# Performance work log

Measured on AMD Instinct MI355X. Metric: run time of the kernel, lower is better.

## Reference

```python
import jax, jax.numpy as jnp
import numpy as np
from functools import partial

DT = 0.1
EPS_RES = 0.01
EIG_MIN = 0.1
EIG_CLIP = 0.99
CHUNK = 128

B, T, D, K = 8, 4096, 1024, 256


def setup_inputs() -> dict:
    key = jax.random.key(0)
    k1, k2, k3, k4, k5 = jax.random.split(key, 5)
    x = jax.random.normal(k1, (B, T, D), dtype=jnp.float32)
    # paper init: alpha ~ U(-3, 0)
    alpha_raw = -3.0 * jax.random.uniform(k2, (K,), dtype=jnp.float32)
    # omega_k = 2*pi*k/K
    omega = 2.0 * jnp.pi * jnp.arange(K, dtype=jnp.float32) / K
    W_in = jax.random.normal(k3, (K, D), dtype=jnp.float32) / np.sqrt(D)
    W_out = jax.random.normal(k4, (D, K), dtype=jnp.float32) / np.sqrt(K)
    M = jax.random.normal(k5, (K, K), dtype=jnp.float32)
    return {"x": x, "alpha_raw": alpha_raw, "omega": omega,
            "W_in": W_in, "W_out": W_out, "M": M}


def _forward(x, alpha_raw, omega, W_in, W_out, M):
    Bb, Tt, Dd = x.shape
    Kk = alpha_raw.shape[0]
    n_chunks = Tt // CHUNK

    # eigenvalue magnitude/phase with constraints
    mag = EIG_MIN + jax.nn.sigmoid(alpha_raw) * (EIG_CLIP - EIG_MIN)     # (K,)
    cos_p = jnp.cos(omega * DT)
    sin_p = jnp.sin(omega * DT)
    # resonance R = I + eps * M / ||M||_F
    R = jnp.eye(Kk, dtype=x.dtype) + EPS_RES * M / (jnp.linalg.norm(M) + 1e-8)

    # parallel input projection for all timesteps: (B,T,K)
    beta = jnp.einsum('btd,kd->btk', x, W_in)
    # (n_chunks, CHUNK, B, K) for scanning over chunks then timesteps
    beta_c = jnp.transpose(beta.reshape(Bb, n_chunks, CHUNK, Kk), (1, 2, 0, 3))

    def time_step(carry, b):
        r, i = carry                                     # (B,K) each
        nr = b + mag * (r * cos_p - i * sin_p)           # beta added to real only
        ni = mag * (r * sin_p + i * cos_p)
        return (nr, ni), (nr, ni)

    def chunk_step(carry, beta_ch):
        # beta_ch: (CHUNK, B, K)
        (_, _), (ar, ai) = jax.lax.scan(time_step, carry, beta_ch)
        # resonance coupling applied to every state of the chunk
        ar = ar @ R
        ai = ai @ R
        # state handed to next chunk is the resonance-coupled last state,
        # detached at the chunk boundary (as in the original training scheme)
        new_carry = (jax.lax.stop_gradient(ar[-1]), jax.lax.stop_gradient(ai[-1]))
        return new_carry, ar

    zero = jnp.zeros((Bb, Kk), dtype=x.dtype)
    _, states_real = jax.lax.scan(chunk_step, (zero, zero), beta_c)
    # states_real: (n_chunks, CHUNK, B, K) -> (B, T, K)
    states_real = jnp.transpose(states_real, (2, 0, 1, 3)).reshape(Bb, Tt, Kk)

    # parallel output projection (dropout is identity in eval)
    out = jnp.einsum('btk,dk->btd', states_real, W_out)
    return out


@jax.jit
def reference(x, alpha_raw, omega, W_in, W_out, M):
    return _forward(x, alpha_raw, omega, W_in, W_out, M)
```

## Files before the change

kernel.cpp:

```cpp
#include <hip/hip_runtime.h>
#include <math.h>


typedef __attribute__((ext_vector_type(8))) short short8;
typedef __attribute__((ext_vector_type(4))) float f32x4;

#define EPS_RES 0.01f

union U8 { unsigned u[4]; short8 s8; };

__device__ __forceinline__ unsigned short f2bf(float f) {
  unsigned u = __float_as_uint(f) + 0x8000u;
  return (unsigned short)(u >> 16);
}
__device__ __forceinline__ float bf2f(unsigned short h) {
  return __uint_as_float(((unsigned)h) << 16);
}
__device__ __forceinline__ unsigned pk2bf(float f0, float f1) {
  return __builtin_amdgcn_perm(__float_as_uint(f1) + 0x8000u,
                               __float_as_uint(f0) + 0x8000u, 0x07060302u);
}
__device__ __forceinline__ void gl_lds16(const void* g, void* l) {
  __builtin_amdgcn_global_load_lds(
      (const __attribute__((address_space(1))) unsigned*)g,
      (__attribute__((address_space(3))) unsigned*)l, 16, 0, 0);
}

__global__ __launch_bounds__(256) void k_setup(const float* __restrict__ M,
                                               float* __restrict__ part,
                                               const float* __restrict__ W,
                                               unsigned short* __restrict__ o) {
  const int bid = blockIdx.x;
  if (bid < 64) {
    const int i = (bid * 256 + threadIdx.x) * 4;
    const float4 v = *(const float4*)(M + i);
    float s = v.x * v.x + v.y * v.y + v.z * v.z + v.w * v.w;
    #pragma unroll
    for (int off = 32; off > 0; off >>= 1) s += __shfl_down(s, off);
    __shared__ float red[4];
    const int lane = threadIdx.x & 63, wv = threadIdx.x >> 6;
    if (lane == 0) red[wv] = s;
    __syncthreads();
    if (threadIdx.x == 0)
      part[bid] = red[0] + red[1] + red[2] + red[3];
  } else {
    const int i = ((bid - 64) * 256 + threadIdx.x) * 4;
    float4 v = *(const float4*)(W + i);
    uint2 p;
    p.x = pk2bf(v.x, v.y);
    p.y = pk2bf(v.z, v.w);
    *(uint2*)(o + i) = p;
  }
}

__device__ __forceinline__ float norm_scale(const float* __restrict__ part) {
  float nsum = 0.f;
  #pragma unroll
  for (int i = 0; i < 64; ++i) nsum += part[i];
  return EPS_RES / (sqrtf(nsum) + 1e-8f);
}

__global__ __launch_bounds__(256) void k_wcomb(const float* __restrict__ Wout,
                                               const float* __restrict__ Mm,
                                               const float* __restrict__ npart,
                                               unsigned short* __restrict__ WcT) {
  const int d0 = blockIdx.x * 8;
  const int k = threadIdx.x;
  __shared__ float wl[8][256];
  #pragma unroll
  for (int dd = 0; dd < 8; ++dd) wl[dd][k] = Wout[(size_t)(d0 + dd) * 256 + k];
  __syncthreads();
  float acc[8] = {0.f, 0.f, 0.f, 0.f, 0.f, 0.f, 0.f, 0.f};
  const float4* Mr = (const float4*)(Mm + (size_t)k * 256);
  for (int j4 = 0; j4 < 64; ++j4) {
    const float4 m4 = Mr[j4];
    #pragma unroll
    for (int dd = 0; dd < 8; ++dd) {
      acc[dd] = fmaf(m4.x, wl[dd][j4 * 4 + 0], acc[dd]);
      acc[dd] = fmaf(m4.y, wl[dd][j4 * 4 + 1], acc[dd]);
      acc[dd] = fmaf(m4.z, wl[dd][j4 * 4 + 2], acc[dd]);
      acc[dd] = fmaf(m4.w, wl[dd][j4 * 4 + 3], acc[dd]);
    }
  }
  const float s = norm_scale(npart);
  #pragma unroll
  for (int dd = 0; dd < 8; ++dd)
    WcT[(size_t)(d0 + dd) * 256 + k] =
        f2bf(Wout[(size_t)(d0 + dd) * 256 + k] + s * acc[dd]);
}

__global__ __launch_bounds__(256) void k_gemm1(const float* __restrict__ A,
                                               const unsigned short* __restrict__ Bw,
                                               float* __restrict__ C) {
  __shared__ __align__(16) float lA[3][64 * 32];
  __shared__ __align__(16) unsigned short lB[3][256 * 32];
  const int tid = threadIdx.x;
  const int wv = tid >> 6, lane = tid & 63;
  const int m0 = blockIdx.x * 64;
  const int wn = wv;
  const int lrow = lane & 15, q = lane >> 4;

  const int a_r8 = lane >> 3;
  const int a_gl = (lane & 7) ^ a_r8;
  const int b_r16 = lane >> 2;
  const int b_gl = (lane & 3) ^ ((b_r16 >> 1) & 3);

  const float* Ab = A + (size_t)(m0 + wv * 16 + a_r8) * 1024 + a_gl * 4;
  const unsigned short* Bb = Bw + (size_t)(wv * 64 + b_r16) * 1024 + b_gl * 8;

  f32x4 acc[4][4] = {};

  auto stage = [&](int bf, int k0) {
    #pragma unroll
    for (int j = 0; j < 2; ++j)
      gl_lds16(Ab + (size_t)j * 8 * 1024 + k0,
               &lA[bf][(wv * 16 + j * 8) * 32]);
    #pragma unroll
    for (int j = 0; j < 4; ++j)
      gl_lds16(Bb + (size_t)j * 16 * 1024 + k0,
               &lB[bf][(wv * 64 + j * 16) * 32]);
  };

  auto compute = [&](int cur) {
    short8 af[4], bfv[4];
    #pragma unroll
    for (int t = 0; t < 4; ++t) {
      const int ra = t * 16 + lrow, sw = ra & 7;
      const float4 lo = *(const float4*)&lA[cur][ra * 32 + (((2 * q) ^ sw) << 2)];
      const float4 hi = *(const float4*)&lA[cur][ra * 32 + (((2 * q + 1) ^ sw) << 2)];
      U8 u;
      u.u[0] = pk2bf(lo.x, lo.y);
      u.u[1] = pk2bf(lo.z, lo.w);
      u.u[2] = pk2bf(hi.x, hi.y);
      u.u[3] = pk2bf(hi.z, hi.w);
      af[t] = u.s8;
      const int rb = wn * 64 + t * 16 + lrow;
      bfv[t] = *(const short8*)&lB[cur][rb * 32 + (q ^ ((rb >> 1) & 3)) * 8];
    }
    #pragma unroll
    for (int tm = 0; tm < 4; ++tm)
      #pragma unroll
      for (int tn = 0; tn < 4; ++tn)
        acc[tm][tn] = __builtin_amdgcn_mfma_f32_16x16x32_bf16(
            af[tm], bfv[tn], acc[tm][tn], 0, 0, 0);
  };

  stage(0, 0);
  stage(1, 32);
  int cur = 0;
  for (int j = 0; j < 31; ++j) {
    asm volatile("s_waitcnt vmcnt(6)" ::: "memory");
    __builtin_amdgcn_s_barrier();
    if (j + 2 < 32) {
      const int nx = (cur + 2 >= 3) ? cur - 1 : cur + 2;
      stage(nx, (j + 2) * 32);
    }
    compute(cur);
    cur = (cur + 1 >= 3) ? 0 : cur + 1;
  }
  asm volatile("s_waitcnt vmcnt(0)" ::: "memory");
  __builtin_amdgcn_s_barrier();
  compute(cur);

  const int rbase = m0 + q * 4;
  const int cbase = wn * 64 + lrow;
  #pragma unroll
  for (int tm = 0; tm < 4; ++tm)
    #pragma unroll
    for (int tn = 0; tn < 4; ++tn)
      #pragma unroll
      for (int r = 0; r < 4; ++r)
        C[(size_t)(rbase + tm * 16 + r) * 256 + (cbase + tn * 16)] =
            acc[tm][tn][r];
}

__global__ __launch_bounds__(256) void k_gemm2(const unsigned short* __restrict__ A,
                                               const unsigned short* __restrict__ Bw,
                                               float* __restrict__ C) {
  __shared__ __align__(16) unsigned short lA[3][128 * 32];
  __shared__ __align__(16) unsigned short lB[3][128 * 32];
  const int tid = threadIdx.x;
  const int wv = tid >> 6, lane = tid & 63;
  const int bid = blockIdx.x + (blockIdx.y << 8);
  const int xcd = bid & 7, ii = bid >> 3;
  const int m0 = ((xcd << 5) + (ii >> 3)) * 128;
  const int n0 = (ii & 7) * 128;
  const int wm = wv & 1, wn = wv >> 1;
  const int lrow = lane & 15, q = lane >> 4;

  const int r16 = lane >> 2;
  const int g4 = (lane & 3) ^ ((r16 >> 1) & 3);

  const unsigned short* Ab = A + (size_t)(m0 + wv * 32 + r16) * 256 + g4 * 8;
  const unsigned short* Bb = Bw + (size_t)(n0 + wv * 32 + r16) * 256 + g4 * 8;

  f32x4 acc[4][4] = {};

  auto stage = [&](int bf, int k0) {
    #pragma unroll
    for (int j = 0; j < 2; ++j) {
      gl_lds16(Ab + (size_t)j * 16 * 256 + k0,
               &lA[bf][(wv * 32 + j * 16) * 32]);
      gl_lds16(Bb + (size_t)j * 16 * 256 + k0,
               &lB[bf][(wv * 32 + j * 16) * 32]);
    }
  };

  auto compute = [&](int cur) {
    short8 af[4], bfv[4];
    #pragma unroll
    for (int t = 0; t < 4; ++t) {
      const int ra = wm * 64 + t * 16 + lrow;
      af[t] = *(const short8*)&lA[cur][ra * 32 + ((q ^ ((ra >> 1) & 3)) << 3)];
      const int rb = wn * 64 + t * 16 + lrow;
      bfv[t] = *(const short8*)&lB[cur][rb * 32 + ((q ^ ((rb >> 1) & 3)) << 3)];
    }
    #pragma unroll
    for (int tm = 0; tm < 4; ++tm)
      #pragma unroll
      for (int tn = 0; tn < 4; ++tn)
        acc[tm][tn] = __builtin_amdgcn_mfma_f32_16x16x32_bf16(
            af[tm], bfv[tn], acc[tm][tn], 0, 0, 0);
  };

  stage(0, 0);
  stage(1, 32);
  int cur = 0;
  for (int j = 0; j < 7; ++j) {
    asm volatile("s_waitcnt vmcnt(4)" ::: "memory");
    __builtin_amdgcn_s_barrier();
    if (j + 2 < 8) {
      const int nx = (cur + 2 >= 3) ? cur - 1 : cur + 2;
      stage(nx, (j + 2) * 32);
    }
    compute(cur);
    cur = (cur + 1 >= 3) ? 0 : cur + 1;
  }
  asm volatile("s_waitcnt vmcnt(0)" ::: "memory");
  __builtin_amdgcn_s_barrier();
  compute(cur);

  const int rbase = m0 + wm * 64 + (lane >> 4) * 4;
  const int cbase = n0 + wn * 64 + (lane & 15);
  #pragma unroll
  for (int tm = 0; tm < 4; ++tm)
    #pragma unroll
    for (int tn = 0; tn < 4; ++tn)
      #pragma unroll
      for (int r = 0; r < 4; ++r)
        C[(size_t)(rbase + tm * 16 + r) * 1024 + (cbase + tn * 16)] =
            acc[tm][tn][r];
}

__global__ __launch_bounds__(256) void k_scan(const float* __restrict__ beta,
                                              unsigned short* __restrict__ rez,
                                              float* __restrict__ lastR,
                                              float* __restrict__ lastI,
                                              const float* __restrict__ alpha_raw,
                                              const float* __restrict__ omega) {
  const int c = blockIdx.x & 31, b = blockIdx.x >> 5;
  const int k = threadIdx.x;
  const float a = alpha_raw[k];
  const float sig = 1.f / (1.f + expf(-a));
  const float mag = 0.1f + sig * (0.99f - 0.1f);
  const float om = omega[k] * 0.1f;
  const float lc = mag * cosf(om), ls = mag * sinf(om);

  const size_t m0 = (size_t)b * 4096 + (size_t)c * 128;
  const float* bp = beta + m0 * 256 + k;
  unsigned short* rp = rez + m0 * 256 + k;
  float r = 0.f, im = 0.f;
  #pragma unroll 8
  for (int t = 0; t < 128; ++t) {
    float be = bp[(size_t)t * 256];
    float nr = fmaf(lc, r, fmaf(-ls, im, be));
    float ni = fmaf(ls, r, lc * im);
    r = nr; im = ni;
    rp[(size_t)t * 256] = f2bf(r);
  }
  const int idx = (c * 8 + b) * 256 + k;
  lastR[idx] = r;
  lastI[idx] = im;
}

__global__ __launch_bounds__(256) void k_carry(const float* __restrict__ lastR,
                                               const float* __restrict__ lastI,
                                               const float* __restrict__ Mm,
                                               const float* __restrict__ npart,
                                               float* __restrict__ carR,
                                               float* __restrict__ carI) {
  const int c = blockIdx.x & 31, b = blockIdx.x >> 5;
  const int j = threadIdx.x;
  const int oidx = (c * 8 + b) * 256 + j;
  if (c == 0) {
    carR[oidx] = 0.f;
    carI[oidx] = 0.f;
    return;
  }
  __shared__ float lr[256], li[256];
  const int iidx = ((c - 1) * 8 + b) * 256;
  lr[j] = lastR[iidx + j];
  li[j] = lastI[iidx + j];
  __syncthreads();
  float ar = 0.f, ai = 0.f;
  for (int kk = 0; kk < 256; ++kk) {
    float m = Mm[(size_t)kk * 256 + j];
    ar = fmaf(lr[kk], m, ar);
    ai = fmaf(li[kk], m, ai);
  }
  const float s = norm_scale(npart);
  carR[oidx] = lr[j] + s * ar;
  carI[oidx] = li[j] + s * ai;
}

__global__ __launch_bounds__(256) void k_fixup(unsigned short* __restrict__ rez,
                                               const float* __restrict__ carR,
                                               const float* __restrict__ carI,
                                               const float* __restrict__ alpha_raw,
                                               const float* __restrict__ omega) {
  const int tg = blockIdx.x & 7;
  const int cb = blockIdx.x >> 3;
  const int b = cb & 7, c = (cb >> 3) + 1;
  const int k = threadIdx.x;
  const float a = alpha_raw[k];
  const float sig = 1.f / (1.f + expf(-a));
  const float mag = 0.1f + sig * (0.99f - 0.1f);
  const float om = omega[k] * 0.1f;
  const float l2m = log2f(mag);

  const float cr = carR[(c * 8 + b) * 256 + k];
  const float ci = carI[(c * 8 + b) * 256 + k];
  unsigned short* rp =
      rez + ((size_t)b * 4096 + (size_t)c * 128 + tg * 8) * 256 + k;
  #pragma unroll
  for (int tt = 0; tt < 8; ++tt) {
    const float tp1 = (float)(tg * 8 + tt + 1);
    const float p = exp2f(tp1 * l2m);
    const float ang = tp1 * om;
    const float hr = p * (cosf(ang) * cr - sinf(ang) * ci);
    rp[(size_t)tt * 256] = f2bf(bf2f(rp[(size_t)tt * 256]) + hr);
  }
}

extern "C" void kernel_launch(void* const* d_in, const int* in_sizes, int n_in,
                              void* d_out, int out_size, void* d_ws,
                              size_t ws_size, hipStream_t stream) {
  const float* x         = (const float*)d_in[0];
  const float* alpha_raw = (const float*)d_in[1];
  const float* omega     = (const float*)d_in[2];
  const float* W_in      = (const float*)d_in[3];
  const float* W_out     = (const float*)d_in[4];
  const float* Mm        = (const float*)d_in[5];
  float* out = (float*)d_out;

  char* ws = (char*)d_ws;
  float*          beta  = (float*)(ws);
  unsigned short* rez   = (unsigned short*)(ws + 33554432);
  float*          lastR = (float*)(ws + 50331648);
  float*          lastI = (float*)(ws + 50331648 + 262144);
  float*          carR  = (float*)(ws + 50331648 + 2 * 262144);
  float*          carI  = (float*)(ws + 50331648 + 3 * 262144);
  unsigned short* WcT   = (unsigned short*)(ws + 50331648 + 4 * 262144);
  float*          npart = (float*)(ws + 50331648 + 4 * 262144 + 524288);
  unsigned short* WinT  = (unsigned short*)d_out;

  k_setup<<<320, 256, 0, stream>>>(Mm, npart, W_in, WinT);
  k_wcomb<<<128, 256, 0, stream>>>(W_out, Mm, npart, WcT);
  k_gemm1<<<512, 256, 0, stream>>>(x, WinT, beta);
  k_scan<<<256, 256, 0, stream>>>(beta, rez, lastR, lastI, alpha_raw, omega);
  k_carry<<<256, 256, 0, stream>>>(lastR, lastI, Mm, npart, carR, carI);
  k_fixup<<<1984, 256, 0, stream>>>(rez, carR, carI, alpha_raw, omega);
  k_gemm2<<<dim3(256, 8), 256, 0, stream>>>(rez, WcT, out);
}
```

Baseline: 329.7 us.

## Load GEMM B operand directly from global and double-buffer A with wider K tiles

Both projection GEMMs stop staging the weight (B) operand through shared memory and instead read its MFMA fragments straight from global memory into registers. Only the A operand is still staged, now double-buffered with a 64-wide K slice instead of triple-buffered 32-wide slices. Synchronisation becomes a plain __syncthreads per step instead of hand-tuned vmcnt waits. This cuts LDS footprint and LDS traffic, which may raise occupancy, but exposes B global-load latency in the MFMA loop and reduces prefetch depth.

Result: no change. 334.5 us (+1.4%).

```diff
diff --git a/kernel.cpp b/kernel.cpp
--- a/kernel.cpp
+++ b/kernel.cpp
@@ -92,75 +92,65 @@
 __global__ __launch_bounds__(256) void k_gemm1(const float* __restrict__ A,
                                                const unsigned short* __restrict__ Bw,
                                                float* __restrict__ C) {
-  __shared__ __align__(16) float lA[3][64 * 32];
-  __shared__ __align__(16) unsigned short lB[3][256 * 32];
+  __shared__ __align__(16) float lA[2][64 * 64];
   const int tid = threadIdx.x;
   const int wv = tid >> 6, lane = tid & 63;
   const int m0 = blockIdx.x * 64;
   const int wn = wv;
   const int lrow = lane & 15, q = lane >> 4;
 
-  const int a_r8 = lane >> 3;
-  const int a_gl = (lane & 7) ^ a_r8;
-  const int b_r16 = lane >> 2;
-  const int b_gl = (lane & 3) ^ ((b_r16 >> 1) & 3);
-
-  const float* Ab = A + (size_t)(m0 + wv * 16 + a_r8) * 1024 + a_gl * 4;
-  const unsigned short* Bb = Bw + (size_t)(wv * 64 + b_r16) * 1024 + b_gl * 8;
+  const int s_r4 = lane >> 4;
+
+  const unsigned short* Bt[4];
+  #pragma unroll
+  for (int t = 0; t < 4; ++t)
+    Bt[t] = Bw + (size_t)(wn * 64 + t * 16 + lrow) * 1024 + q * 8;
 
   f32x4 acc[4][4] = {};
 
   auto stage = [&](int bf, int k0) {
     #pragma unroll
-    for (int j = 0; j < 2; ++j)
-      gl_lds16(Ab + (size_t)j * 8 * 1024 + k0,
-               &lA[bf][(wv * 16 + j * 8) * 32]);
-    #pragma unroll
-    for (int j = 0; j < 4; ++j)
-      gl_lds16(Bb + (size_t)j * 16 * 1024 + k0,
-               &lB[bf][(wv * 64 + j * 16) * 32]);
+    for (int j = 0; j < 4; ++j) {
+      const int rloc = j * 4 + s_r4;
+      const int g = (lane & 15) ^ rloc;
+      gl_lds16(A + (size_t)(m0 + wv * 16 + rloc) * 1024 + k0 + g * 4,
+               &lA[bf][(wv * 16 + j * 4) * 64]);
+    }
   };
 
-  auto compute = [&](int cur) {
-    short8 af[4], bfv[4];
-    #pragma unroll
-    for (int t = 0; t < 4; ++t) {
-      const int ra = t * 16 + lrow, sw = ra & 7;
-      const float4 lo = *(const float4*)&lA[cur][ra * 32 + (((2 * q) ^ sw) << 2)];
-      const float4 hi = *(const float4*)&lA[cur][ra * 32 + (((2 * q + 1) ^ sw) << 2)];
-      U8 u;
-      u.u[0] = pk2bf(lo.x, lo.y);
-      u.u[1] = pk2bf(lo.z, lo.w);
-      u.u[2] = pk2bf(hi.x, hi.y);
-      u.u[3] = pk2bf(hi.z, hi.w);
-      af[t] = u.s8;
-      const int rb = wn * 64 + t * 16 + lrow;
-      bfv[t] = *(const short8*)&lB[cur][rb * 32 + (q ^ ((rb >> 1) & 3)) * 8];
-    }
-    #pragma unroll
-    for (int tm = 0; tm < 4; ++tm)
-      #pragma unroll
-      for (int tn = 0; tn < 4; ++tn)
-        acc[tm][tn] = __builtin_amdgcn_mfma_f32_16x16x32_bf16(
-            af[tm], bfv[tn], acc[tm][tn], 0, 0, 0);
-  };
-
   stage(0, 0);
-  stage(1, 32);
-  int cur = 0;
-  for (int j = 0; j < 31; ++j) {
-    asm volatile("s_waitcnt vmcnt(6)" ::: "memory");
-    __builtin_amdgcn_s_barrier();
-    if (j + 2 < 32) {
-      const int nx = (cur + 2 >= 3) ? cur - 1 : cur + 2;
-      stage(nx, (j + 2) * 32);
-    }
-    compute(cur);
-    cur = (cur + 1 >= 3) ? 0 : cur + 1;
-  }
-  asm volatile("s_waitcnt vmcnt(0)" ::: "memory");
-  __builtin_amdgcn_s_barrier();
-  compute(cur);
+  for (int s = 0; s < 16; ++s) {
+    const int cur = s & 1;
+    __syncthreads();
+    if (s + 1 < 16) stage(cur ^ 1, (s + 1) * 64);
+
+    #pragma unroll
+    for (int ks = 0; ks < 2; ++ks) {
+      short8 af[4], bfv[4];
+      #pragma unroll
+      for (int t = 0; t < 4; ++t) {
+        const int ra = t * 16 + lrow;
+        const int g0 = ks * 8 + 2 * q;
+        const float4 lo =
+            *(const float4*)&lA[cur][ra * 64 + ((g0 ^ (ra & 15)) << 2)];
+        const float4 hi =
+            *(const float4*)&lA[cur][ra * 64 + (((g0 + 1) ^ (ra & 15)) << 2)];
+        U8 u;
+        u.u[0] = pk2bf(lo.x, lo.y);
+        u.u[1] = pk2bf(lo.z, lo.w);
+        u.u[2] = pk2bf(hi.x, hi.y);
+        u.u[3] = pk2bf(hi.z, hi.w);
+        af[t] = u.s8;
+        bfv[t] = *(const short8*)(Bt[t] + s * 64 + ks * 32);
+      }
+      #pragma unroll
+      for (int tm = 0; tm < 4; ++tm)
+        #pragma unroll
+        for (int tn = 0; tn < 4; ++tn)
+          acc[tm][tn] = __builtin_amdgcn_mfma_f32_16x16x32_bf16(
+              af[tm], bfv[tn], acc[tm][tn], 0, 0, 0);
+    }
+  }
 
   const int rbase = m0 + q * 4;
   const int cbase = wn * 64 + lrow;
@@ -177,8 +167,7 @@
 __global__ __launch_bounds__(256) void k_gemm2(const unsigned short* __restrict__ A,
                                                const unsigned short* __restrict__ Bw,
                                                float* __restrict__ C) {
-  __shared__ __align__(16) unsigned short lA[3][128 * 32];
-  __shared__ __align__(16) unsigned short lB[3][128 * 32];
+  __shared__ __align__(16) unsigned short lA[2][128 * 64];
   const int tid = threadIdx.x;
   const int wv = tid >> 6, lane = tid & 63;
   const int bid = blockIdx.x + (blockIdx.y << 8);
@@ -188,57 +177,49 @@
   const int wm = wv & 1, wn = wv >> 1;
   const int lrow = lane & 15, q = lane >> 4;
 
-  const int r16 = lane >> 2;
-  const int g4 = (lane & 3) ^ ((r16 >> 1) & 3);
-
-  const unsigned short* Ab = A + (size_t)(m0 + wv * 32 + r16) * 256 + g4 * 8;
-  const unsigned short* Bb = Bw + (size_t)(n0 + wv * 32 + r16) * 256 + g4 * 8;
+  const int s_r8 = lane >> 3;
+
+  const unsigned short* Bt[4];
+  #pragma unroll
+  for (int t = 0; t < 4; ++t)
+    Bt[t] = Bw + (size_t)(n0 + wn * 64 + t * 16 + lrow) * 256 + q * 8;
 
   f32x4 acc[4][4] = {};
 
   auto stage = [&](int bf, int k0) {
     #pragma unroll
-    for (int j = 0; j < 2; ++j) {
-      gl_lds16(Ab + (size_t)j * 16 * 256 + k0,
-               &lA[bf][(wv * 32 + j * 16) * 32]);
-      gl_lds16(Bb + (size_t)j * 16 * 256 + k0,
-               &lB[bf][(wv * 32 + j * 16) * 32]);
+    for (int j = 0; j < 4; ++j) {
+      const int rloc = j * 8 + s_r8;
+      const int g = (lane & 7) ^ (rloc & 7);
+      gl_lds16(A + (size_t)(m0 + wv * 32 + rloc) * 256 + k0 + g * 8,
+               &lA[bf][(wv * 32 + j * 8) * 64]);
     }
   };
 
-  auto compute = [&](int cur) {
-    short8 af[4], bfv[4];
-    #pragma unroll
-    for (int t = 0; t < 4; ++t) {
-      const int ra = wm * 64 + t * 16 + lrow;
-      af[t] = *(const short8*)&lA[cur][ra * 32 + ((q ^ ((ra >> 1) & 3)) << 3)];
-      const int rb = wn * 64 + t * 16 + lrow;
-      bfv[t] = *(const short8*)&lB[cur][rb * 32 + ((q ^ ((rb >> 1) & 3)) << 3)];
-    }
-    #pragma unroll
-    for (int tm = 0; tm < 4; ++tm)
-      #pragma unroll
-      for (int tn = 0; tn < 4; ++tn)
-        acc[tm][tn] = __builtin_amdgcn_mfma_f32_16x16x32_bf16(
-            af[tm], bfv[tn], acc[tm][tn], 0, 0, 0);
-  };
-
   stage(0, 0);
-  stage(1, 32);
-  int cur = 0;
-  for (int j = 0; j < 7; ++j) {
-    asm volatile("s_waitcnt vmcnt(4)" ::: "memory");
-    __builtin_amdgcn_s_barrier();
-    if (j + 2 < 8) {
-      const int nx = (cur + 2 >= 3) ? cur - 1 : cur + 2;
-      stage(nx, (j + 2) * 32);
-    }
-    compute(cur);
-    cur = (cur + 1 >= 3) ? 0 : cur + 1;
-  }
-  asm volatile("s_waitcnt vmcnt(0)" ::: "memory");
-  __builtin_amdgcn_s_barrier();
-  compute(cur);
+  for (int s = 0; s < 4; ++s) {
+    const int cur = s & 1;
+    __syncthreads();
+    if (s + 1 < 4) stage(cur ^ 1, (s + 1) * 64);
+
+    #pragma unroll
+    for (int ks = 0; ks < 2; ++ks) {
+      short8 af[4], bfv[4];
+      #pragma unroll
+      for (int t = 0; t < 4; ++t) {
+        const int ra = wm * 64 + t * 16 + lrow;
+        af[t] = *(const short8*)
+            &lA[cur][ra * 64 + (((ks * 4 + q) ^ (ra & 7)) << 3)];
+        bfv[t] = *(const short8*)(Bt[t] + s * 64 + ks * 32);
+      }
+      #pragma unroll
+      for (int tm = 0; tm < 4; ++tm)
+        #pragma unroll
+        for (int tn = 0; tn < 4; ++tn)
+          acc[tm][tn] = __builtin_amdgcn_mfma_f32_16x16x32_bf16(
+              af[tm], bfv[tn], acc[tm][tn], 0, 0, 0);
+    }
+  }
 
   const int rbase = m0 + wm * 64 + (lane >> 4) * 4;
   const int cbase = n0 + wn * 64 + (lane & 15);
```

## Fuse intra-chunk scan into input-projection GEMM epilogue via LDS staging

Applied to the files above, without the earlier changes.

The input-projection GEMM now computes 128x128 tiles, one per (batch, chunk, half-K), and stages the accumulator tile in shared memory. The first 128 threads then run the 128-step recurrence directly from LDS and write bf16 states plus the last states. This removes the separate scan kernel and the 32 MB fp32 beta round trip through global memory. In exchange the scan epilogue runs on only half the block's threads while the other half sit idle, and the larger tile changes occupancy and LDS use (72 KB per block).

New measurement: 320.0 us. 1.03x faster.

```diff
diff --git a/kernel.cpp b/kernel.cpp
--- a/kernel.cpp
+++ b/kernel.cpp
@@ -91,13 +91,18 @@
 
 __global__ __launch_bounds__(256) void k_gemm1(const float* __restrict__ A,
                                                const unsigned short* __restrict__ Bw,
-                                               float* __restrict__ C) {
-  __shared__ __align__(16) float lA[3][64 * 32];
-  __shared__ __align__(16) unsigned short lB[3][256 * 32];
+                                               unsigned short* __restrict__ rez,
+                                               float* __restrict__ lastR,
+                                               float* __restrict__ lastI,
+                                               const float* __restrict__ alpha_raw,
+                                               const float* __restrict__ omega) {
+  __shared__ __align__(16) char arena[73728];
   const int tid = threadIdx.x;
   const int wv = tid >> 6, lane = tid & 63;
-  const int m0 = blockIdx.x * 64;
-  const int wn = wv;
+  const int mt = blockIdx.x >> 1;
+  const int n0 = (blockIdx.x & 1) * 128;
+  const int m0 = mt * 128;
+  const int wm = wv & 1, wn = wv >> 1;
   const int lrow = lane & 15, q = lane >> 4;
 
   const int a_r8 = lane >> 3;
@@ -105,29 +110,33 @@
   const int b_r16 = lane >> 2;
   const int b_gl = (lane & 3) ^ ((b_r16 >> 1) & 3);
 
-  const float* Ab = A + (size_t)(m0 + wv * 16 + a_r8) * 1024 + a_gl * 4;
-  const unsigned short* Bb = Bw + (size_t)(wv * 64 + b_r16) * 1024 + b_gl * 8;
+  const float* Ab = A + (size_t)(m0 + wv * 32 + a_r8) * 1024 + a_gl * 4;
+  const unsigned short* Bb =
+      Bw + (size_t)(n0 + wv * 32 + b_r16) * 1024 + b_gl * 8;
 
   f32x4 acc[4][4] = {};
 
   auto stage = [&](int bf, int k0) {
+    float* la = (float*)(arena + bf * 16384);
+    unsigned short* lb = (unsigned short*)(arena + 49152 + bf * 8192);
+    #pragma unroll
+    for (int j = 0; j < 4; ++j)
+      gl_lds16(Ab + (size_t)j * 8 * 1024 + k0, &la[(wv * 32 + j * 8) * 32]);
     #pragma unroll
     for (int j = 0; j < 2; ++j)
-      gl_lds16(Ab + (size_t)j * 8 * 1024 + k0,
-               &lA[bf][(wv * 16 + j * 8) * 32]);
-    #pragma unroll
-    for (int j = 0; j < 4; ++j)
-      gl_lds16(Bb + (size_t)j * 16 * 1024 + k0,
-               &lB[bf][(wv * 64 + j * 16) * 32]);
+      gl_lds16(Bb + (size_t)j * 16 * 1024 + k0, &lb[(wv * 32 + j * 16) * 32]);
   };
 
   auto compute = [&](int cur) {
+    const float* la = (const float*)(arena + cur * 16384);
+    const unsigned short* lb =
+        (const unsigned short*)(arena + 49152 + cur * 8192);
     short8 af[4], bfv[4];
     #pragma unroll
     for (int t = 0; t < 4; ++t) {
-      const int ra = t * 16 + lrow, sw = ra & 7;
-      const float4 lo = *(const float4*)&lA[cur][ra * 32 + (((2 * q) ^ sw) << 2)];
-      const float4 hi = *(const float4*)&lA[cur][ra * 32 + (((2 * q + 1) ^ sw) << 2)];
+      const int ra = wm * 64 + t * 16 + lrow, sw = ra & 7;
+      const float4 lo = *(const float4*)&la[ra * 32 + (((2 * q) ^ sw) << 2)];
+      const float4 hi = *(const float4*)&la[ra * 32 + (((2 * q + 1) ^ sw) << 2)];
       U8 u;
       u.u[0] = pk2bf(lo.x, lo.y);
       u.u[1] = pk2bf(lo.z, lo.w);
@@ -135,7 +144,7 @@
       u.u[3] = pk2bf(hi.z, hi.w);
       af[t] = u.s8;
       const int rb = wn * 64 + t * 16 + lrow;
-      bfv[t] = *(const short8*)&lB[cur][rb * 32 + (q ^ ((rb >> 1) & 3)) * 8];
+      bfv[t] = *(const short8*)&lb[rb * 32 + (q ^ ((rb >> 1) & 3)) * 8];
     }
     #pragma unroll
     for (int tm = 0; tm < 4; ++tm)
@@ -147,31 +156,52 @@
 
   stage(0, 0);
   stage(1, 32);
-  int cur = 0;
   for (int j = 0; j < 31; ++j) {
     asm volatile("s_waitcnt vmcnt(6)" ::: "memory");
     __builtin_amdgcn_s_barrier();
-    if (j + 2 < 32) {
-      const int nx = (cur + 2 >= 3) ? cur - 1 : cur + 2;
-      stage(nx, (j + 2) * 32);
-    }
-    compute(cur);
-    cur = (cur + 1 >= 3) ? 0 : cur + 1;
+    if (j + 2 < 32) stage((j + 2) % 3, (j + 2) * 32);
+    compute(j % 3);
   }
   asm volatile("s_waitcnt vmcnt(0)" ::: "memory");
   __builtin_amdgcn_s_barrier();
-  compute(cur);
-
-  const int rbase = m0 + q * 4;
-  const int cbase = wn * 64 + lrow;
+  compute(31 % 3);
+
+  __syncthreads();
+  float* accL = (float*)arena;
+  const int colb = wn * 64 + lrow;
   #pragma unroll
   for (int tm = 0; tm < 4; ++tm)
     #pragma unroll
     for (int tn = 0; tn < 4; ++tn)
       #pragma unroll
       for (int r = 0; r < 4; ++r)
-        C[(size_t)(rbase + tm * 16 + r) * 256 + (cbase + tn * 16)] =
+        accL[(wm * 64 + tm * 16 + q * 4 + r) * 132 + colb + tn * 16] =
             acc[tm][tn][r];
+  __syncthreads();
+
+  if (tid < 128) {
+    const int k = n0 + tid;
+    const float a = alpha_raw[k];
+    const float sig = 1.f / (1.f + expf(-a));
+    const float mag = 0.1f + sig * (0.99f - 0.1f);
+    const float om = omega[k] * 0.1f;
+    const float lc = mag * cosf(om), ls = mag * sinf(om);
+
+    unsigned short* rp = rez + (size_t)m0 * 256 + k;
+    float r = 0.f, im = 0.f;
+    #pragma unroll 8
+    for (int t = 0; t < 128; ++t) {
+      float be = accL[t * 132 + tid];
+      float nr = fmaf(lc, r, fmaf(-ls, im, be));
+      float ni = fmaf(ls, r, lc * im);
+      r = nr; im = ni;
+      rp[(size_t)t * 256] = f2bf(r);
+    }
+    const int c = mt & 31, b = mt >> 5;
+    const int idx = (c * 8 + b) * 256 + k;
+    lastR[idx] = r;
+    lastI[idx] = im;
+  }
 }
 
 __global__ __launch_bounds__(256) void k_gemm2(const unsigned short* __restrict__ A,
@@ -225,20 +255,15 @@
 
   stage(0, 0);
   stage(1, 32);
-  int cur = 0;
   for (int j = 0; j < 7; ++j) {
     asm volatile("s_waitcnt vmcnt(4)" ::: "memory");
     __builtin_amdgcn_s_barrier();
-    if (j + 2 < 8) {
-      const int nx = (cur + 2 >= 3) ? cur - 1 : cur + 2;
-      stage(nx, (j + 2) * 32);
-    }
-    compute(cur);
-    cur = (cur + 1 >= 3) ? 0 : cur + 1;
+    if (j + 2 < 8) stage((j + 2) % 3, (j + 2) * 32);
+    compute(j % 3);
   }
   asm volatile("s_waitcnt vmcnt(0)" ::: "memory");
   __builtin_amdgcn_s_barrier();
-  compute(cur);
+  compute(7 % 3);
 
   const int rbase = m0 + wm * 64 + (lane >> 4) * 4;
   const int cbase = n0 + wn * 64 + (lane & 15);
@@ -250,37 +275,6 @@
       for (int r = 0; r < 4; ++r)
         C[(size_t)(rbase + tm * 16 + r) * 1024 + (cbase + tn * 16)] =
             acc[tm][tn][r];
-}
-
-__global__ __launch_bounds__(256) void k_scan(const float* __restrict__ beta,
-                                              unsigned short* __restrict__ rez,
-                                              float* __restrict__ lastR,
-                                              float* __restrict__ lastI,
-                                              const float* __restrict__ alpha_raw,
-                                              const float* __restrict__ omega) {
-  const int c = blockIdx.x & 31, b = blockIdx.x >> 5;
-  const int k = threadIdx.x;
-  const float a = alpha_raw[k];
-  const float sig = 1.f / (1.f + expf(-a));
-  const float mag = 0.1f + sig * (0.99f - 0.1f);
-  const float om = omega[k] * 0.1f;
-  const float lc = mag * cosf(om), ls = mag * sinf(om);
-
-  const size_t m0 = (size_t)b * 4096 + (size_t)c * 128;
-  const float* bp = beta + m0 * 256 + k;
-  unsigned short* rp = rez + m0 * 256 + k;
-  float r = 0.f, im = 0.f;
-  #pragma unroll 8
-  for (int t = 0; t < 128; ++t) {
-    float be = bp[(size_t)t * 256];
-    float nr = fmaf(lc, r, fmaf(-ls, im, be));
-    float ni = fmaf(ls, r, lc * im);
-    r = nr; im = ni;
-    rp[(size_t)t * 256] = f2bf(r);
-  }
-  const int idx = (c * 8 + b) * 256 + k;
-  lastR[idx] = r;
-  lastI[idx] = im;
 }
 
 __global__ __launch_bounds__(256) void k_carry(const float* __restrict__ lastR,
@@ -354,20 +348,19 @@
   float* out = (float*)d_out;
 
   char* ws = (char*)d_ws;
-  float*          beta  = (float*)(ws);
-  unsigned short* rez   = (unsigned short*)(ws + 33554432);
-  float*          lastR = (float*)(ws + 50331648);
-  float*          lastI = (float*)(ws + 50331648 + 262144);
-  float*          carR  = (float*)(ws + 50331648 + 2 * 262144);
-  float*          carI  = (float*)(ws + 50331648 + 3 * 262144);
-  unsigned short* WcT   = (unsigned short*)(ws + 50331648 + 4 * 262144);
-  float*          npart = (float*)(ws + 50331648 + 4 * 262144 + 524288);
+  unsigned short* rez   = (unsigned short*)(ws);
+  float*          lastR = (float*)(ws + 16777216);
+  float*          lastI = (float*)(ws + 16777216 + 262144);
+  float*          carR  = (float*)(ws + 16777216 + 2 * 262144);
+  float*          carI  = (float*)(ws + 16777216 + 3 * 262144);
+  unsigned short* WcT   = (unsigned short*)(ws + 16777216 + 4 * 262144);
+  float*          npart = (float*)(ws + 16777216 + 4 * 262144 + 524288);
   unsigned short* WinT  = (unsigned short*)d_out;
 
   k_setup<<<320, 256, 0, stream>>>(Mm, npart, W_in, WinT);
   k_wcomb<<<128, 256, 0, stream>>>(W_out, Mm, npart, WcT);
-  k_gemm1<<<512, 256, 0, stream>>>(x, WinT, beta);
-  k_scan<<<256, 256, 0, stream>>>(beta, rez, lastR, lastI, alpha_raw, omega);
+  k_gemm1<<<512, 256, 0, stream>>>(x, WinT, rez, lastR, lastI,
+                                   alpha_raw, omega);
   k_carry<<<256, 256, 0, stream>>>(lastR, lastI, Mm, npart, carR, carI);
   k_fixup<<<1984, 256, 0, stream>>>(rez, carR, carI, alpha_raw, omega);
   k_gemm2<<<dim3(256, 8), 256, 0, stream>>>(rez, WcT, out);
```
